# Kernel optimization log

Hardware: AMD Instinct MI355X
Metric: run time of the kernel (lower is better)

## Reference

```python
import jax, jax.numpy as jnp
import numpy as np
import math

DIM, H, Q_RANK, KV_RANK = 2048, 16, 768, 512
QK_STATIC, QK_ROT, V_DIM = 128, 64, 128
QK_TOTAL = QK_STATIC + QK_ROT
BS, SEQ = 2, 1024


def rmsnorm(x, scale, eps=1e-6):
    xf = x.astype(jnp.float32)
    return scale * (xf * jax.lax.rsqrt(jnp.mean(xf * xf, axis=-1, keepdims=True) + eps))


def half_rotate(x):
    h = x.shape[-1] // 2
    return jnp.concatenate([-x[..., h:], x[..., :h]], axis=-1)


def rope_tables(seq_len, dim):
    inv_freq = 1.0 / (10000.0 ** (jnp.arange(0, dim, 2, dtype=jnp.float32) / dim))
    freqs = jnp.arange(seq_len, dtype=jnp.float32)[:, None] * inv_freq[None, :]
    cos = jnp.concatenate([jnp.cos(freqs), jnp.cos(freqs)], axis=-1)  # (S, dim)
    sin = jnp.concatenate([jnp.sin(freqs), jnp.sin(freqs)], axis=-1)
    return cos, sin


def setup_inputs() -> dict:
    key = jax.random.key(0)
    ks = jax.random.split(key, 10)
    sc = lambda fan_in: 1.0 / math.sqrt(fan_in)
    x = jax.random.normal(ks[0], (BS, SEQ, DIM), dtype=jnp.float32)
    causal = jnp.where(jnp.tril(jnp.ones((SEQ, SEQ), dtype=bool)), 0.0, -1e9).astype(jnp.float32)
    mask = jnp.broadcast_to(causal[None], (BS, SEQ, SEQ))
    return {
        "x": x,
        "start_pos": 0,
        "mask": mask,
        "q_down_w": jax.random.normal(ks[1], (Q_RANK, DIM)) * sc(DIM),
        "q_down_b": jnp.zeros((Q_RANK,), jnp.float32),
        "q_norm_scale": jnp.ones((Q_RANK,), jnp.float32),
        "q_up_w": jax.random.normal(ks[2], (H * QK_TOTAL, Q_RANK)) * sc(Q_RANK),
        "q_up_b": jnp.zeros((H * QK_TOTAL,), jnp.float32),
        "kv_down_w": jax.random.normal(ks[3], (KV_RANK + QK_ROT, DIM)) * sc(DIM),
        "kv_down_b": jnp.zeros((KV_RANK + QK_ROT,), jnp.float32),
        "kv_norm_scale": jnp.ones((KV_RANK,), jnp.float32),
        "kv_up_w": jax.random.normal(ks[4], (H * (QK_STATIC + V_DIM), KV_RANK)) * sc(KV_RANK),
        "out_w": jax.random.normal(ks[5], (DIM, H * V_DIM)) * sc(H * V_DIM),
        "out_b": jnp.zeros((DIM,), jnp.float32),
    }


def reference(x, start_pos, mask, q_down_w, q_down_b, q_norm_scale, q_up_w, q_up_b,
              kv_down_w, kv_down_b, kv_norm_scale, kv_up_w, out_w, out_b):
    bs, seq_len, _ = x.shape
    # q path: down-proj -> RMSNorm -> up-proj
    q = rmsnorm(x @ q_down_w.T + q_down_b, q_norm_scale)
    q = (q @ q_up_w.T + q_up_b).reshape(bs, seq_len, H, QK_TOTAL)
    q_static, q_rot = q[..., :QK_STATIC], q[..., QK_STATIC:]
    # kv path: shared down-proj producing latent features + rotary key part
    kv = x @ kv_down_w.T + kv_down_b
    kv_feat, k_rot = kv[..., :KV_RANK], kv[..., KV_RANK:]
    # RoPE (original indexes positions 0..seq_len-1)
    cos, sin = rope_tables(seq_len, QK_ROT)
    q_rot = q_rot * cos[None, :, None, :] + half_rotate(q_rot) * sin[None, :, None, :]
    k_rot = k_rot * cos[None, :, :] + half_rotate(k_rot) * sin[None, :, :]  # (b, t, r)
    kv_normed = rmsnorm(kv_feat, kv_norm_scale)  # latent cache contents (b, t, c)
    # matrix absorption: fold kv_up key-weights into q
    w_k_abs = kv_up_w[: H * QK_STATIC, :].reshape(H, QK_STATIC, KV_RANK)
    w_v_abs = kv_up_w[-H * V_DIM :, :].reshape(H, V_DIM, KV_RANK)
    q_static_proj = jnp.einsum('bshd,hdc->bshc', q_static, w_k_abs)
    attn_scores = (jnp.einsum('bshc,btc->bsht', q_static_proj, kv_normed)
                   + jnp.einsum('bshr,btr->bsht', q_rot, k_rot)) / math.sqrt(QK_TOTAL)
    attn_scores = attn_scores + mask[:, :, None, :]
    attn_weights = jax.nn.softmax(attn_scores, axis=-1)
    # attend over latent features, then expand with absorbed value weights
    ctx_c = jnp.einsum('bsht,btc->bshc', attn_weights, kv_normed)
    ctx = jnp.einsum('bshc,hdc->bshd', ctx_c, w_v_abs)
    out = ctx.reshape(bs, seq_len, H * V_DIM) @ out_w.T + out_b
    return out
```

## Files before the change

### kernel.cpp

```cpp
#include <hip/hip_runtime.h>
#include <stdint.h>
#include <stddef.h>


typedef __attribute__((ext_vector_type(8))) short bf16x8;
typedef __attribute__((ext_vector_type(4))) float f32x4;

__device__ inline float b2f(unsigned short v){
    union { unsigned u; float f; } x; x.u = ((unsigned)v) << 16; return x.f;
}
__device__ inline unsigned short f2b(float f){
    union { float f; unsigned u; } x; x.f = f;
    unsigned r = x.u + 0x7fffu + ((x.u >> 16) & 1u);
    return (unsigned short)(r >> 16);
}

__device__ __forceinline__ void gl2lds16(const unsigned short* g, unsigned short* l){
    __builtin_amdgcn_global_load_lds(
        (__attribute__((address_space(1))) void*)const_cast<unsigned short*>(g),
        (__attribute__((address_space(3))) void*)l,
        16, 0, 0);
}

template<typename TC>
static __device__ __forceinline__ void gemm_body(
    unsigned short (*As)[4096], unsigned short (*Bs)[4096],
    const unsigned short* A, const unsigned short* B,
    const float* bias, TC* C,
    int N, int K, int lda, int ldb, int ldc,
    int m0, int n0, float alpha, int causal)
{
    const int tid = threadIdx.x, w = tid >> 6, lane = tid & 63;
    const int wm = w >> 1, wn = w & 1;

    const int srow = w * 32 + (lane >> 2);
    const int schunk = ((lane & 3) ^ ((lane >> 3) & 3)) * 8;
    const unsigned short* gA = A + (size_t)(m0 + srow) * lda + schunk;
    const unsigned short* gB = B + (size_t)(n0 + srow) * ldb + schunk;

    const int ktiles = K >> 5;
    auto stage = [&](int buf, int kt){
        const int k0 = kt << 5;
        gl2lds16(gA + k0,            &As[buf][w * 1024]);
        gl2lds16(gA + k0 + 16 * lda, &As[buf][w * 1024 + 512]);
        gl2lds16(gB + k0,            &Bs[buf][w * 1024]);
        gl2lds16(gB + k0 + 16 * ldb, &Bs[buf][w * 1024 + 512]);
    };
    stage(0, 0);
    if (ktiles > 1) stage(1, 1);

    f32x4 acc[4][4] = {};
    const int lm = lane & 15;
    const int kq = (((lane >> 4) ^ (lm >> 1)) & 3) * 8;

    int cur = 0;
    for (int kt = 0; kt < ktiles; ++kt){
        if (kt + 1 < ktiles) __builtin_amdgcn_s_waitcnt(0xF74);
        else                 __builtin_amdgcn_s_waitcnt(0xF70);
        __builtin_amdgcn_s_barrier();
        __asm__ volatile("" ::: "memory");
        if (kt + 2 < ktiles) stage(cur >= 1 ? cur - 1 : 2, kt + 2);
        bf16x8 af[4], bfr[4];
        #pragma unroll
        for (int i = 0; i < 4; ++i)
            af[i] = *(const bf16x8*)&As[cur][(wm * 64 + i * 16 + lm) * 32 + kq];
        #pragma unroll
        for (int j = 0; j < 4; ++j)
            bfr[j] = *(const bf16x8*)&Bs[cur][(wn * 64 + j * 16 + lm) * 32 + kq];
        #pragma unroll
        for (int i = 0; i < 4; ++i)
            #pragma unroll
            for (int j = 0; j < 4; ++j)
                acc[i][j] = __builtin_amdgcn_mfma_f32_16x16x32_bf16(af[i], bfr[j], acc[i][j], 0, 0, 0);
        __asm__ volatile("" ::: "memory");
        cur = (cur == 2) ? 0 : cur + 1;
    }

    #pragma unroll
    for (int i = 0; i < 4; ++i){
        const int m = m0 + wm * 64 + i * 16 + (lane >> 4) * 4;
        #pragma unroll
        for (int j = 0; j < 4; ++j){
            const int n = n0 + wn * 64 + j * 16 + lm;
            if (n < N){
                const float bb = bias ? bias[n] : 0.f;
                #pragma unroll
                for (int r = 0; r < 4; ++r){
                    float v = acc[i][j][r] * alpha + bb;
                    if ((causal & 1) && n > m + r) v = -1e9f;
                    if constexpr (sizeof(TC) == 2)
                        C[(size_t)(m + r) * ldc + n] = (TC)f2b(v);
                    else
                        C[(size_t)(m + r) * ldc + n] = (TC)v;
                }
            }
        }
    }
}

template<typename TC>
__global__ __launch_bounds__(256) void mfma_gemm_bt(
    const unsigned short* __restrict__ A, const unsigned short* __restrict__ B,
    const float* __restrict__ bias, TC* __restrict__ C,
    int M, int N, int K, int lda, int ldb, int ldc,
    int zdiv, long sA_hi, long sA_lo, long sB_hi, long sB_lo, long sC_hi, long sC_lo,
    float alpha, int causal)
{
    int z, bm, bn;
    if (causal & 4){ z = blockIdx.x; bm = blockIdx.y; bn = blockIdx.z; }
    else           { z = blockIdx.z; bm = blockIdx.y; bn = blockIdx.x; }
    int m0, n0;
    if (causal & 1){
        int i = bm;
        int mt = (int)((sqrtf(8.f * i + 1.f) - 1.f) * 0.5f);
        while ((mt + 1) * (mt + 2) / 2 <= i) ++mt;
        while (mt * (mt + 1) / 2 > i) --mt;
        n0 = (i - mt * (mt + 1) / 2) * 128;
        m0 = mt * 128;
    } else { m0 = bm * 128; n0 = bn * 128; }
    if (causal & 2) K = min(K, m0 + 128);

    __shared__ unsigned short As[3][4096];
    __shared__ unsigned short Bs[3][4096];
    const int zh = z / zdiv, zl = z % zdiv;
    A += (size_t)zh * sA_hi + (size_t)zl * sA_lo;
    B += (size_t)zh * sB_hi + (size_t)zl * sB_lo;
    C += (size_t)zh * sC_hi + (size_t)zl * sC_lo;

    gemm_body<TC>(As, Bs, A, B, bias, C, N, K, lda, ldb, ldc, m0, n0, alpha, causal);
}

__global__ __launch_bounds__(256) void mfma_gemm_vk(
    const unsigned short* __restrict__ kvuw,
    const unsigned short* __restrict__ kcat,
    unsigned short* __restrict__ vhT,
    unsigned short* __restrict__ khcat)
{
    __shared__ unsigned short As[3][4096];
    __shared__ unsigned short Bs[3][4096];
    const int p = blockIdx.x & 1, z = blockIdx.x >> 1, y = blockIdx.y;
    const int b = z >> 4, h = z & 15;
    if (p == 0){
        const unsigned short* A = kvuw + 1048576 + (size_t)h * 65536;
        const unsigned short* B = kcat + (size_t)b * 589824;
        unsigned short* C = vhT + (size_t)b * 2097152 + (size_t)h * 131072;
        gemm_body<unsigned short>(As, Bs, A, B, nullptr, C,
                                  1024, 512, 512, 576, 1024, 0, y * 128, 1.0f, 0);
    } else {
        const unsigned short* A = kcat + (size_t)b * 589824;
        const unsigned short* B = kvuw + (size_t)h * 65536;
        unsigned short* C = khcat + (size_t)b * 3145728 + (size_t)h * 196608;
        gemm_body<unsigned short>(As, Bs, A, B, nullptr, C,
                                  128, 512, 576, 512, 192, y * 128, 0, 1.0f, 0);
    }
}

__global__ __launch_bounds__(256) void flash_attn(
    const unsigned short* __restrict__ qu,
    const unsigned short* __restrict__ khcat,
    const unsigned short* __restrict__ vhT,
    unsigned short* __restrict__ ctx)
{
    const int t = blockIdx.x;
    const int k15 = t & 15, kl = k15 & 7;
    int v = (kl & 1) ? (1 + (kl >> 1)) : (8 - (kl >> 1));
    if (k15 & 8) v = 9 - v;
    if (t & 256) v = 9 - v;
    const int o = ((t >> 4) & 15) * 2 + (k15 >> 3) + ((t >> 8) << 5);
    const int mt = 2 * v - 2 + (o & 1);
    const int z  = o >> 1;
    const int b = z >> 4, h = z & 15;
    const int m0 = mt * 64;
    const int nkt = v;

    __shared__ char smem[74240];
    unsigned short (*Qs)[4096] = (unsigned short (*)[4096])smem;
    unsigned short (*Ks)[8192] = (unsigned short (*)[8192])(smem + 24576);
    unsigned short* Ps = (unsigned short*)(smem + 24576);
    float* lrow = (float*)(smem + 73728);

    const unsigned short* kB = khcat + (size_t)z * 196608;
    const unsigned short* vB = vhT + (size_t)z * 131072;

    const int tid = threadIdx.x, w = tid >> 6, lane = tid & 63;
    const int wm = w >> 1, wn = w & 1;
    const int lm = lane & 15, g = lane >> 4;
    const int kq = g * 8;
    const int rs7 = lm & 7;

    if (tid < 128) lrow[tid] = 0.f;

    const int srow8 = lane >> 3;
    const int soff8 = ((lane & 7) ^ (lane >> 3)) * 8;
    const unsigned short* gQ = qu + (size_t)(b * 1024 + m0 + w * 16 + srow8) * 3072
                               + h * 192 + soff8;

    #pragma unroll
    for (int c = 0; c < 3; ++c){
        gl2lds16(gQ + c * 64,            &Qs[c][w * 1024]);
        gl2lds16(gQ + c * 64 + 8 * 3072, &Qs[c][w * 1024 + 512]);
    }

    auto stageK = [&](int buf, int kt, int c){
        const unsigned short* gK = kB + (size_t)(kt * 128 + w * 32 + srow8) * 192
                                   + c * 64 + soff8;
        gl2lds16(gK,            &Ks[buf][w * 2048]);
        gl2lds16(gK + 8 * 192,  &Ks[buf][w * 2048 + 512]);
        gl2lds16(gK + 16 * 192, &Ks[buf][w * 2048 + 1024]);
        gl2lds16(gK + 24 * 192, &Ks[buf][w * 2048 + 1536]);
    };
    stageK(2, 0, 0);

    f32x4 Oacc[2][4] = {};
    const float scl = 0.07216878364870322f;

    for (int kt = 0; kt < nkt; ++kt){
        stageK(0, kt, 1);
        stageK(1, kt, 2);
        __asm__ volatile("" ::: "memory");
        bf16x8 vfr[4][4];
        #pragma unroll
        for (int j = 0; j < 4; ++j)
            #pragma unroll
            for (int kc = 0; kc < 4; ++kc)
                vfr[j][kc] = *(const bf16x8*)(vB + (size_t)(wn * 64 + j * 16 + lm) * 1024
                                              + kt * 128 + kc * 32 + kq);
        __asm__ volatile("" ::: "memory");

        f32x4 S[2][4] = {};
        #pragma unroll
        for (int c = 0; c < 3; ++c){
            if      (c == 0) __builtin_amdgcn_s_waitcnt(0x4F78);
            else if (c == 1) __builtin_amdgcn_s_waitcnt(0x4F74);
            else             __builtin_amdgcn_s_waitcnt(0x4F70);
            __builtin_amdgcn_s_barrier();
            __asm__ volatile("" ::: "memory");
            const int bufc = (c == 0) ? 2 : (c - 1);
            bf16x8 af[2][2], bfr[4][2];
            #pragma unroll
            for (int i = 0; i < 2; ++i)
                #pragma unroll
                for (int kk = 0; kk < 2; ++kk)
                    af[i][kk] = *(const bf16x8*)&Qs[c][(wm * 32 + i * 16 + lm) * 64
                                                       + (((kk * 4 + g) ^ rs7) * 8)];
            #pragma unroll
            for (int j = 0; j < 4; ++j)
                #pragma unroll
                for (int kk = 0; kk < 2; ++kk)
                    bfr[j][kk] = *(const bf16x8*)&Ks[bufc][(wn * 64 + j * 16 + lm) * 64
                                                           + (((kk * 4 + g) ^ rs7) * 8)];
            __builtin_amdgcn_s_setprio(1);
            #pragma unroll
            for (int kk = 0; kk < 2; ++kk)
                #pragma unroll
                for (int i = 0; i < 2; ++i)
                    #pragma unroll
                    for (int j = 0; j < 4; ++j)
                        S[i][j] = __builtin_amdgcn_mfma_f32_16x16x32_bf16(af[i][kk], bfr[j][kk], S[i][j], 0, 0, 0);
            __builtin_amdgcn_s_setprio(0);
            __asm__ volatile("" ::: "memory");
        }
        __builtin_amdgcn_s_waitcnt(0xC07F);
        __builtin_amdgcn_s_barrier();
        __asm__ volatile("" ::: "memory");
        if (kt + 1 < nkt) stageK(2, kt + 1, 0);

        const bool diag = (kt == (mt >> 1));
        #pragma unroll
        for (int i = 0; i < 2; ++i){
            float rs[4] = {0.f, 0.f, 0.f, 0.f};
            #pragma unroll
            for (int j = 0; j < 4; ++j){
                const int nloc = wn * 64 + j * 16 + lm;
                #pragma unroll
                for (int r = 0; r < 4; ++r){
                    const int mloc = wm * 32 + i * 16 + g * 4 + r;
                    float p = __expf(S[i][j][r] * scl);
                    if (diag && (kt * 128 + nloc) > (m0 + mloc)) p = 0.f;
                    rs[r] += p;
                    Ps[mloc * 136 + nloc] = f2b(p);
                }
            }
            #pragma unroll
            for (int r = 0; r < 4; ++r){
                rs[r] += __shfl_xor(rs[r], 1, 64);
                rs[r] += __shfl_xor(rs[r], 2, 64);
                rs[r] += __shfl_xor(rs[r], 4, 64);
                rs[r] += __shfl_xor(rs[r], 8, 64);
            }
            if (lm == 0){
                #pragma unroll
                for (int r = 0; r < 4; ++r)
                    lrow[wn * 64 + wm * 32 + i * 16 + g * 4 + r] += rs[r];
            }
        }
        __asm__ volatile("" ::: "memory");
        __builtin_amdgcn_s_waitcnt(0xC07F);
        __builtin_amdgcn_s_barrier();
        __asm__ volatile("" ::: "memory");

        if (kt + 1 < nkt) __builtin_amdgcn_s_waitcnt(0xF74);
        else              __builtin_amdgcn_s_waitcnt(0xF70);
        #pragma unroll
        for (int kc = 0; kc < 4; ++kc){
            bf16x8 pa[2];
            #pragma unroll
            for (int i = 0; i < 2; ++i)
                pa[i] = *(const bf16x8*)&Ps[(wm * 32 + i * 16 + lm) * 136 + kc * 32 + kq];
            __builtin_amdgcn_s_setprio(1);
            #pragma unroll
            for (int i = 0; i < 2; ++i)
                #pragma unroll
                for (int j = 0; j < 4; ++j)
                    Oacc[i][j] = __builtin_amdgcn_mfma_f32_16x16x32_bf16(pa[i], vfr[j][kc], Oacc[i][j], 0, 0, 0);
            __builtin_amdgcn_s_setprio(0);
        }
        __asm__ volatile("" ::: "memory");
        __builtin_amdgcn_s_waitcnt(0xC07F);
        __builtin_amdgcn_s_barrier();
        __asm__ volatile("" ::: "memory");
    }

    unsigned short* cBase = ctx + ((size_t)(b * 1024 + m0)) * 2048 + h * 128;
    #pragma unroll
    for (int i = 0; i < 2; ++i){
        #pragma unroll
        for (int r = 0; r < 4; ++r){
            const int row = wm * 32 + i * 16 + g * 4 + r;
            const float inv = 1.f / (lrow[row] + lrow[64 + row]);
            #pragma unroll
            for (int j = 0; j < 4; ++j){
                const int col = wn * 64 + j * 16 + lm;
                cBase[(size_t)row * 2048 + col] = f2b(Oacc[i][j][r] * inv);
            }
        }
    }
}

__global__ __launch_bounds__(256) void cast_all(
    const float* __restrict__ s0, unsigned short* __restrict__ d0,
    const float* __restrict__ s1, unsigned short* __restrict__ d1,
    const float* __restrict__ s2, unsigned short* __restrict__ d2,
    const float* __restrict__ s3, unsigned short* __restrict__ d3,
    const float* __restrict__ s4, unsigned short* __restrict__ d4,
    const float* __restrict__ s5, unsigned short* __restrict__ d5)
{
    long i = (long)(blockIdx.x * 256 + threadIdx.x) * 4;
    const float* s; unsigned short* d; long off;
    if      (i <  4194304L){ s = s0; d = d0; off = i; }
    else if (i <  5767168L){ s = s1; d = d1; off = i -  4194304L; }
    else if (i <  8126464L){ s = s2; d = d2; off = i -  5767168L; }
    else if (i <  9306112L){ s = s3; d = d3; off = i -  8126464L; }
    else if (i < 11403264L){ s = s4; d = d4; off = i -  9306112L; }
    else                   { s = s5; d = d5; off = i - 11403264L; }
    float4 v = *(const float4*)(s + off);
    *(ushort4*)(d + off) = make_ushort4(f2b(v.x), f2b(v.y), f2b(v.z), f2b(v.w));
}

__global__ __launch_bounds__(256) void fused_down_post(
    const unsigned short* __restrict__ p,
    const float* __restrict__ q_down_b, const float* __restrict__ kv_down_b,
    const float* __restrict__ q_norm_s, const float* __restrict__ kv_norm_s,
    unsigned short* __restrict__ qn, unsigned short* __restrict__ kcat)
{
    __shared__ float row[1344];
    __shared__ float red[4];
    const int t = blockIdx.x, tid = threadIdx.x;
    const long S = 2752512L;
    const unsigned short* b0 = p + (size_t)t * 1344;
    for (int c = tid; c < 1344; c += 256){
        float v = b2f(b0[c]) + b2f(b0[c + S]) + b2f(b0[c + 2*S]) + b2f(b0[c + 3*S]);
        v += (c < 768) ? q_down_b[c] : kv_down_b[c - 768];
        row[c] = v;
    }
    __syncthreads();
    const int lane = tid & 63, w = tid >> 6;
    float ss = 0.f;
    for (int c = tid; c < 768; c += 256){ float v = row[c]; ss += v * v; }
    #pragma unroll
    for (int o = 32; o > 0; o >>= 1) ss += __shfl_xor(ss, o, 64);
    if (lane == 0) red[w] = ss;
    __syncthreads();
    const float inv1 = rsqrtf((red[0]+red[1]+red[2]+red[3]) / 768.f + 1e-6f);
    __syncthreads();
    ss = 0.f;
    for (int c = tid; c < 512; c += 256){ float v = row[768 + c]; ss += v * v; }
    #pragma unroll
    for (int o = 32; o > 0; o >>= 1) ss += __shfl_xor(ss, o, 64);
    if (lane == 0) red[w] = ss;
    __syncthreads();
    const float inv2 = rsqrtf((red[0]+red[1]+red[2]+red[3]) / 512.f + 1e-6f);
    for (int c = tid; c < 768; c += 256)
        qn[(size_t)t * 768 + c] = f2b(q_norm_s[c] * row[c] * inv1);
    for (int c = tid; c < 512; c += 256)
        kcat[(size_t)t * 576 + c] = f2b(kv_norm_s[c] * row[768 + c] * inv2);
    if (tid < 64){
        const int d = tid, s = t & 1023;
        float x  = row[1280 + d];
        float xp = (d < 32) ? -row[1280 + d + 32] : row[1280 + d - 32];
        float ang = (float)s * powf(10000.f, -(float)(2 * (d & 31)) / 64.f);
        kcat[(size_t)t * 576 + 512 + d] = f2b(x * cosf(ang) + xp * sinf(ang));
    }
}

__global__ __launch_bounds__(256) void rope_q_krot(
    unsigned short* __restrict__ qu,
    const unsigned short* __restrict__ kcat,
    unsigned short* __restrict__ khcat)
{
    long idx = (long)blockIdx.x * 256 + threadIdx.x;
    if (idx < 1048576L){
        const int d   = idx & 31;
        const int h   = (idx >> 5) & 15;
        const int tok = idx >> 9;
        const int s   = tok & 1023;
        unsigned short* base = qu + (size_t)tok * 3072 + h * 192 + 128;
        float x1 = b2f(base[d]), x2 = b2f(base[d + 32]);
        float ang = (float)s * powf(10000.f, -(float)d / 32.f);
        float c = cosf(ang), sn = sinf(ang);
        base[d]      = f2b(x1 * c - x2 * sn);
        base[d + 32] = f2b(x2 * c + x1 * sn);
    } else {
        idx -= 1048576L;
        const int d   = idx & 63;
        const int h   = (idx >> 6) & 15;
        const int tok = (int)(idx >> 10);
        const int bb  = tok >> 10, s = tok & 1023;
        khcat[((size_t)(bb * 16 + h) * 1024 + s) * 192 + 128 + d] =
            kcat[(size_t)tok * 576 + 512 + d];
    }
}

extern "C" void kernel_launch(void* const* d_in, const int* in_sizes, int n_in,
                              void* d_out, int out_size, void* d_ws, size_t ws_size,
                              hipStream_t stream)
{
    const float* x         = (const float*)d_in[0];
    const float* q_down_w  = (const float*)d_in[3];
    const float* q_down_b  = (const float*)d_in[4];
    const float* q_norm_s  = (const float*)d_in[5];
    const float* q_up_w    = (const float*)d_in[6];
    const float* q_up_b    = (const float*)d_in[7];
    const float* kv_down_w = (const float*)d_in[8];
    const float* kv_down_b = (const float*)d_in[9];
    const float* kv_norm_s = (const float*)d_in[10];
    const float* kv_up_w   = (const float*)d_in[11];
    const float* out_w     = (const float*)d_in[12];
    const float* out_b     = (const float*)d_in[13];
    float* out = (float*)d_out;

    char* ws = (char*)d_ws;
    unsigned short* kvuw  = (unsigned short*)(ws + 0);
    unsigned short* outw  = (unsigned short*)(ws + 4194304);
    unsigned short* kcat  = (unsigned short*)(ws + 12582912);
    unsigned short* vhT   = (unsigned short*)(ws + 14942208);
    unsigned short* khcat = (unsigned short*)(ws + 23330816);
    unsigned short* ctx   = (unsigned short*)(ws + 35913728);
    unsigned short* qu    = (unsigned short*)(ws + 44302336);
    unsigned short* qn    = (unsigned short*)(ws + 56885248);
    unsigned short* p_qkv = (unsigned short*)(ws + 60030976);
    unsigned short* xb    = (unsigned short*)(ws + 82051072);
    unsigned short* qkdw  = (unsigned short*)(ws + 90439680);
    unsigned short* quw   = (unsigned short*)(ws + 96206848);

    dim3 blk(256);

    cast_all<<<15232, blk, 0, stream>>>(x, xb, q_down_w, qkdw, q_up_w, quw,
                                        kv_down_w, qkdw + 1572864, kv_up_w, kvuw, out_w, outw);

    mfma_gemm_bt<unsigned short><<<dim3(11, 16, 4), blk, 0, stream>>>(
        xb, qkdw, nullptr, p_qkv, 2048, 1344, 512, 2048, 2048, 1344,
        4, 0L, 512L, 0L, 512L, 0L, 2752512L, 1.0f, 0);
    fused_down_post<<<2048, blk, 0, stream>>>(p_qkv, q_down_b, kv_down_b,
                                              q_norm_s, kv_norm_s, qn, kcat);
    mfma_gemm_bt<unsigned short><<<dim3(24, 16, 1), blk, 0, stream>>>(
        qn, quw, q_up_b, qu, 2048, 3072, 768, 768, 768, 3072,
        1, 0, 0, 0, 0, 0, 0, 1.0f, 0);
    mfma_gemm_vk<<<dim3(64, 8, 1), blk, 0, stream>>>(kvuw, kcat, vhT, khcat);
    rope_q_krot<<<12288, blk, 0, stream>>>(qu, kcat, khcat);
    flash_attn<<<dim3(512), blk, 0, stream>>>(qu, khcat, vhT, ctx);
    mfma_gemm_bt<float><<<dim3(16, 16, 1), blk, 0, stream>>>(
        ctx, outw, out_b, out, 2048, 2048, 2048, 2048, 2048, 2048,
        1, 0L, 0L, 0L, 0L, 0L, 0L, 1.0f, 0);
}
```

Baseline: 293.4 us.

## Split-K output projection with bf16 partials and reorder flash-attn block scheduling

The output projection GEMM is split along K into two halves, doubling the grid so more blocks run concurrently. Each half writes bf16 partials, and a new reduce kernel sums them, adds the bias and writes fp32 output. The flash-attention block-to-tile mapping is also replaced with a simpler heavy-first ordering (longest causal rows first, then shortest) to improve load balance across CUs. Rounding partials to bf16 before the sum adds precision loss, and the extra kernel launch plus partial traffic add overhead.

```diff
diff --git a/kernel.cpp b/kernel.cpp
--- a/kernel.cpp
+++ b/kernel.cpp
@@ -162,16 +162,13 @@
     unsigned short* __restrict__ ctx)
 {
     const int t = blockIdx.x;
-    const int k15 = t & 15, kl = k15 & 7;
-    int v = (kl & 1) ? (1 + (kl >> 1)) : (8 - (kl >> 1));
-    if (k15 & 8) v = 9 - v;
-    if (t & 256) v = 9 - v;
-    const int o = ((t >> 4) & 15) * 2 + (k15 >> 3) + ((t >> 8) << 5);
-    const int mt = 2 * v - 2 + (o & 1);
-    const int z  = o >> 1;
+    const int r = t & 7, q = t >> 3;
+    const int z = r + 8 * (q & 3);
+    const int u = q >> 2;
+    const int mt = (u < 8) ? (15 - 2 * u) : (2 * (u - 8));
     const int b = z >> 4, h = z & 15;
     const int m0 = mt * 64;
-    const int nkt = v;
+    const int nkt = (mt >> 1) + 1;
 
     __shared__ char smem[74240];
     unsigned short (*Qs)[4096] = (unsigned short (*)[4096])smem;
@@ -273,25 +270,25 @@
             for (int j = 0; j < 4; ++j){
                 const int nloc = wn * 64 + j * 16 + lm;
                 #pragma unroll
-                for (int r = 0; r < 4; ++r){
-                    const int mloc = wm * 32 + i * 16 + g * 4 + r;
-                    float p = __expf(S[i][j][r] * scl);
+                for (int r2 = 0; r2 < 4; ++r2){
+                    const int mloc = wm * 32 + i * 16 + g * 4 + r2;
+                    float p = __expf(S[i][j][r2] * scl);
                     if (diag && (kt * 128 + nloc) > (m0 + mloc)) p = 0.f;
-                    rs[r] += p;
+                    rs[r2] += p;
                     Ps[mloc * 136 + nloc] = f2b(p);
                 }
             }
             #pragma unroll
-            for (int r = 0; r < 4; ++r){
-                rs[r] += __shfl_xor(rs[r], 1, 64);
-                rs[r] += __shfl_xor(rs[r], 2, 64);
-                rs[r] += __shfl_xor(rs[r], 4, 64);
-                rs[r] += __shfl_xor(rs[r], 8, 64);
+            for (int r2 = 0; r2 < 4; ++r2){
+                rs[r2] += __shfl_xor(rs[r2], 1, 64);
+                rs[r2] += __shfl_xor(rs[r2], 2, 64);
+                rs[r2] += __shfl_xor(rs[r2], 4, 64);
+                rs[r2] += __shfl_xor(rs[r2], 8, 64);
             }
             if (lm == 0){
                 #pragma unroll
-                for (int r = 0; r < 4; ++r)
-                    lrow[wn * 64 + wm * 32 + i * 16 + g * 4 + r] += rs[r];
+                for (int r2 = 0; r2 < 4; ++r2)
+                    lrow[wn * 64 + wm * 32 + i * 16 + g * 4 + r2] += rs[r2];
             }
         }
         __asm__ volatile("" ::: "memory");
@@ -325,13 +322,13 @@
     #pragma unroll
     for (int i = 0; i < 2; ++i){
         #pragma unroll
-        for (int r = 0; r < 4; ++r){
-            const int row = wm * 32 + i * 16 + g * 4 + r;
+        for (int r2 = 0; r2 < 4; ++r2){
+            const int row = wm * 32 + i * 16 + g * 4 + r2;
             const float inv = 1.f / (lrow[row] + lrow[64 + row]);
             #pragma unroll
             for (int j = 0; j < 4; ++j){
                 const int col = wn * 64 + j * 16 + lm;
-                cBase[(size_t)row * 2048 + col] = f2b(Oacc[i][j][r] * inv);
+                cBase[(size_t)row * 2048 + col] = f2b(Oacc[i][j][r2] * inv);
             }
         }
     }
@@ -403,6 +400,20 @@
     }
 }
 
+__global__ __launch_bounds__(256) void reduce_out(
+    const unsigned short* __restrict__ p, const float* __restrict__ bias,
+    float* __restrict__ out)
+{
+    const long S = 4194304L;
+    long i = (long)(blockIdx.x * 256 + threadIdx.x) * 4;
+    ushort4 a = *(const ushort4*)(p + i);
+    ushort4 b = *(const ushort4*)(p + i + S);
+    float4 bb = *(const float4*)(bias + (i & 2047));
+    float4 r = make_float4(b2f(a.x) + b2f(b.x) + bb.x, b2f(a.y) + b2f(b.y) + bb.y,
+                           b2f(a.z) + b2f(b.z) + bb.z, b2f(a.w) + b2f(b.w) + bb.w);
+    *(float4*)(out + i) = r;
+}
+
 __global__ __launch_bounds__(256) void rope_q_krot(
     unsigned short* __restrict__ qu,
     const unsigned short* __restrict__ kcat,
@@ -459,6 +470,7 @@
     unsigned short* qu    = (unsigned short*)(ws + 44302336);
     unsigned short* qn    = (unsigned short*)(ws + 56885248);
     unsigned short* p_qkv = (unsigned short*)(ws + 60030976);
+    unsigned short* p_out = (unsigned short*)(ws + 60030976);
     unsigned short* xb    = (unsigned short*)(ws + 82051072);
     unsigned short* qkdw  = (unsigned short*)(ws + 90439680);
     unsigned short* quw   = (unsigned short*)(ws + 96206848);
@@ -479,7 +491,8 @@
     mfma_gemm_vk<<<dim3(64, 8, 1), blk, 0, stream>>>(kvuw, kcat, vhT, khcat);
     rope_q_krot<<<12288, blk, 0, stream>>>(qu, kcat, khcat);
     flash_attn<<<dim3(512), blk, 0, stream>>>(qu, khcat, vhT, ctx);
-    mfma_gemm_bt<float><<<dim3(16, 16, 1), blk, 0, stream>>>(
-        ctx, outw, out_b, out, 2048, 2048, 2048, 2048, 2048, 2048,
-        1, 0L, 0L, 0L, 0L, 0L, 0L, 1.0f, 0);
-}
+    mfma_gemm_bt<unsigned short><<<dim3(16, 16, 2), blk, 0, stream>>>(
+        ctx, outw, nullptr, p_out, 2048, 2048, 1024, 2048, 2048, 2048,
+        2, 0L, 1024L, 0L, 1024L, 0L, 4194304L, 1.0f, 0);
+    reduce_out<<<4096, blk, 0, stream>>>(p_out, out_b, out);
+}
```

Result: faster. 285.2 us (-2.8%).
